# Performance work log

Measured on AMD Instinct MI355X. Metric: run time of the kernel, lower is better.

## Reference

```python
import jax, jax.numpy as jnp
import numpy as np

N_SAMPLE = 1000
N_LATENT = 64
N_OUT = 64
BATCH = 65536


def setup_inputs() -> dict:
    key = jax.random.key(0)
    k_u, k_sid, k_A, k_off = jax.random.split(key, 4)
    u = jax.random.normal(k_u, (BATCH, N_LATENT), dtype=jnp.float32)
    sample_id = jax.random.randint(k_sid, (BATCH, 1), 0, N_SAMPLE, dtype=jnp.int64)
    amat_sample = jax.random.normal(k_A, (N_SAMPLE, N_LATENT, N_OUT), dtype=jnp.float32)
    offsets = jax.random.normal(k_off, (N_SAMPLE, N_OUT), dtype=jnp.float32)
    return {"u": u, "sample_id": sample_id, "amat_sample": amat_sample, "offsets": offsets}


def reference(u, sample_id, amat_sample, offsets):
    # sample_id: [B, 1] -> [B]
    sid = jnp.squeeze(sample_id, axis=-1).astype(jnp.int32)
    # Gather per-cell decoder matrix: [B, n_latent, n_out]
    As = amat_sample[sid]
    # Original detaches u before the matvec (gradient only flows via residual).
    u_sg = jax.lax.stop_gradient(u)
    # Batched matvec: (As * u[..., None]).sum(-2)
    z2 = jnp.einsum('bd,bdo->bo', u_sg, As)
    delta = z2 + offsets[sid]
    return u + delta
```

## Files before the change

### kernel.cpp

```cpp
#include <hip/hip_runtime.h>
#include <hip/hip_bf16.h>

#define N_LATENT 64
#define N_OUT    64
#define CAP      256
#define CSTRIDE  16
#define NWAVES   5

typedef __attribute__((ext_vector_type(8))) _Float16 f16x8;
typedef __attribute__((ext_vector_type(4))) float    f32x4;

union U4H8 { uint4 u4; f16x8 h8; };

__global__ void build_lists_kernel(const int* __restrict__ sid,
                                   int* __restrict__ cursor,
                                   int* __restrict__ list,
                                   int n4)
{
    const int i = blockIdx.x * blockDim.x + threadIdx.x;
    if (i < n4) {
        const int4 v = ((const int4*)sid)[i];
        int p;
        p = atomicAdd(&cursor[v.x * CSTRIDE], 1); if (p < CAP) list[v.x * CAP + p] = 4 * i;
        p = atomicAdd(&cursor[v.y * CSTRIDE], 1); if (p < CAP) list[v.y * CAP + p] = 4 * i + 1;
        p = atomicAdd(&cursor[v.z * CSTRIDE], 1); if (p < CAP) list[v.z * CAP + p] = 4 * i + 2;
        p = atomicAdd(&cursor[v.w * CSTRIDE], 1); if (p < CAP) list[v.w * CAP + p] = 4 * i + 3;
    }
}

__global__ __launch_bounds__(64 * NWAVES) void decoder_mfma_kernel(
    const float* __restrict__ u,
    const float* __restrict__ amat,
    const float* __restrict__ offsets,
    const int*   __restrict__ cursor,
    const int*   __restrict__ list,
    float*       __restrict__ out)
{
    __shared__ uint Bf[8 * 64 * 4];

    const int s    = blockIdx.x;
    const int tid  = threadIdx.x;
    const int lane = tid & 63;
    const int wave = tid >> 6;

    int n = cursor[s * CSTRIDE];
    n = (n < CAP) ? n : CAP;
    if (n == 0) return;

    const float* __restrict__ Ag  = amat + (size_t)s * (N_LATENT * N_OUT);
    const int*   __restrict__ lst = list + s * CAP;

    for (int c = wave; c < 8; c += NWAVES) {
        const int kk  = c >> 2;
        const int nt  = c & 3;
        const int kb  = kk * 32 + (lane >> 4) * 8;
        const int col = nt * 16 + (lane & 15);
        U4H8 x;
#pragma unroll
        for (int j = 0; j < 8; ++j)
            x.h8[j] = (_Float16)Ag[(kb + j) * N_OUT + col];
        *((uint4*)&Bf[(c * 64 + lane) * 4]) = x.u4;
    }
    __syncthreads();

    const int tiles = (n + 15) >> 4;

    float off_nt[4];
#pragma unroll
    for (int nt = 0; nt < 4; ++nt)
        off_nt[nt] = offsets[(size_t)s * N_OUT + nt * 16 + (lane & 15)];

    for (int t = wave; t < tiles; t += NWAVES) {
        const int ridx = t * 16 + (lane & 15);
        const int brow = lst[(ridx < n) ? ridx : 0];
        const float* __restrict__ up =
            u + (size_t)brow * N_LATENT + ((lane >> 4) * 8);
        f16x8 a0, a1;
        {
            const float4 p0 = *(const float4*)(up);
            const float4 p1 = *(const float4*)(up + 4);
            const float4 p2 = *(const float4*)(up + 32);
            const float4 p3 = *(const float4*)(up + 36);
            a0[0] = (_Float16)p0.x; a0[1] = (_Float16)p0.y;
            a0[2] = (_Float16)p0.z; a0[3] = (_Float16)p0.w;
            a0[4] = (_Float16)p1.x; a0[5] = (_Float16)p1.y;
            a0[6] = (_Float16)p1.z; a0[7] = (_Float16)p1.w;
            a1[0] = (_Float16)p2.x; a1[1] = (_Float16)p2.y;
            a1[2] = (_Float16)p2.z; a1[3] = (_Float16)p2.w;
            a1[4] = (_Float16)p3.x; a1[5] = (_Float16)p3.y;
            a1[6] = (_Float16)p3.z; a1[7] = (_Float16)p3.w;
        }

        int  b2[4]; bool val[4];
#pragma unroll
        for (int r = 0; r < 4; ++r) {
            const int ridx2 = t * 16 + (lane >> 4) * 4 + r;
            val[r] = (ridx2 < n);
            b2[r]  = lst[val[r] ? ridx2 : 0];
        }

#pragma unroll
        for (int nt = 0; nt < 4; ++nt) {
            U4H8 b0, b1;
            b0.u4 = *((const uint4*)&Bf[((0 * 4 + nt) * 64 + lane) * 4]);
            b1.u4 = *((const uint4*)&Bf[((1 * 4 + nt) * 64 + lane) * 4]);
            f32x4 acc = {0.f, 0.f, 0.f, 0.f};
            acc = __builtin_amdgcn_mfma_f32_16x16x32_f16(a0, b0.h8, acc, 0, 0, 0);
            acc = __builtin_amdgcn_mfma_f32_16x16x32_f16(a1, b1.h8, acc, 0, 0, 0);

            const int col = nt * 16 + (lane & 15);
#pragma unroll
            for (int r = 0; r < 4; ++r) {
                if (val[r]) {
                    const size_t idx = (size_t)b2[r] * N_OUT + col;
                    out[idx] = u[idx] + acc[r] + off_nt[nt];
                }
            }
        }
    }
}

extern "C" void kernel_launch(void* const* d_in, const int* in_sizes, int n_in,
                              void* d_out, int out_size, void* d_ws, size_t ws_size,
                              hipStream_t stream)
{
    const float* u       = (const float*)d_in[0];
    const int*   sid     = (const int*)d_in[1];
    const float* amat    = (const float*)d_in[2];
    const float* offsets = (const float*)d_in[3];
    float*       out     = (float*)d_out;

    const int batch    = in_sizes[0] / N_LATENT;
    const int n_sample = in_sizes[2] / (N_LATENT * N_OUT);

    int* cursor = (int*)d_ws;
    int* list   = cursor + (size_t)n_sample * CSTRIDE;

    hipMemsetAsync(cursor, 0, (size_t)n_sample * CSTRIDE * sizeof(int), stream);

    const int n4 = batch / 4;
    build_lists_kernel<<<(n4 + 255) / 256, 256, 0, stream>>>(
        sid, cursor, list, n4);

    decoder_mfma_kernel<<<n_sample, 64 * NWAVES, 0, stream>>>(
        u, amat, offsets, cursor, list, out);
}
```

Baseline: 29.34 us.

## Stage MFMA results in LDS for coalesced float4 epilogue; one id per thread in list build

The MFMA accumulators are written into a per-wave padded LDS tile. The epilogue then reads each output row back as float4 and writes it with coalesced 16-byte loads and stores of u and out, replacing scattered 4-byte accesses. The list-building kernel now handles one sample id per thread instead of four, which spreads the atomics over more threads. The change adds LDS traffic and relies on an lgkmcnt wait with no barrier for intra-wave visibility, which should hold because each wave uses its own tile.

```diff
diff --git a/kernel.cpp b/kernel.cpp
--- a/kernel.cpp
+++ b/kernel.cpp
@@ -6,25 +6,24 @@
 #define CAP      256
 #define CSTRIDE  16
 #define NWAVES   5
+#define TPAD     68
 
 typedef __attribute__((ext_vector_type(8))) _Float16 f16x8;
 typedef __attribute__((ext_vector_type(4))) float    f32x4;
 
 union U4H8 { uint4 u4; f16x8 h8; };
 
-__global__ void build_lists_kernel(const int* __restrict__ sid,
-                                   int* __restrict__ cursor,
-                                   int* __restrict__ list,
-                                   int n4)
+__global__ __launch_bounds__(256) void build_lists_kernel(
+    const int* __restrict__ sid,
+    int* __restrict__ cursor,
+    int* __restrict__ list,
+    int batch)
 {
     const int i = blockIdx.x * blockDim.x + threadIdx.x;
-    if (i < n4) {
-        const int4 v = ((const int4*)sid)[i];
-        int p;
-        p = atomicAdd(&cursor[v.x * CSTRIDE], 1); if (p < CAP) list[v.x * CAP + p] = 4 * i;
-        p = atomicAdd(&cursor[v.y * CSTRIDE], 1); if (p < CAP) list[v.y * CAP + p] = 4 * i + 1;
-        p = atomicAdd(&cursor[v.z * CSTRIDE], 1); if (p < CAP) list[v.z * CAP + p] = 4 * i + 2;
-        p = atomicAdd(&cursor[v.w * CSTRIDE], 1); if (p < CAP) list[v.w * CAP + p] = 4 * i + 3;
+    if (i < batch) {
+        const int s = sid[i];
+        const int p = atomicAdd(&cursor[s * CSTRIDE], 1);
+        if (p < CAP) list[s * CAP + p] = i;
     }
 }
 
@@ -36,7 +35,8 @@
     const int*   __restrict__ list,
     float*       __restrict__ out)
 {
-    __shared__ uint Bf[8 * 64 * 4];
+    __shared__ uint  Bf[8 * 64 * 4];
+    __shared__ float Ot[NWAVES][16 * TPAD];
 
     const int s    = blockIdx.x;
     const int tid  = threadIdx.x;
@@ -65,10 +65,9 @@
 
     const int tiles = (n + 15) >> 4;
 
-    float off_nt[4];
-#pragma unroll
-    for (int nt = 0; nt < 4; ++nt)
-        off_nt[nt] = offsets[(size_t)s * N_OUT + nt * 16 + (lane & 15)];
+    const float4 offv = *(const float4*)(offsets + (size_t)s * N_OUT + (lane & 15) * 4);
+
+    float* __restrict__ myT = &Ot[wave][0];
 
     for (int t = wave; t < tiles; t += NWAVES) {
         const int ridx = t * 16 + (lane & 15);
@@ -91,14 +90,6 @@
             a1[6] = (_Float16)p3.z; a1[7] = (_Float16)p3.w;
         }
 
-        int  b2[4]; bool val[4];
-#pragma unroll
-        for (int r = 0; r < 4; ++r) {
-            const int ridx2 = t * 16 + (lane >> 4) * 4 + r;
-            val[r] = (ridx2 < n);
-            b2[r]  = lst[val[r] ? ridx2 : 0];
-        }
-
 #pragma unroll
         for (int nt = 0; nt < 4; ++nt) {
             U4H8 b0, b1;
@@ -110,11 +101,29 @@
 
             const int col = nt * 16 + (lane & 15);
 #pragma unroll
-            for (int r = 0; r < 4; ++r) {
-                if (val[r]) {
-                    const size_t idx = (size_t)b2[r] * N_OUT + col;
-                    out[idx] = u[idx] + acc[r] + off_nt[nt];
-                }
+            for (int r = 0; r < 4; ++r)
+                myT[((lane >> 4) * 4 + r) * TPAD + col] = acc[r];
+        }
+        asm volatile("s_waitcnt lgkmcnt(0)" ::: "memory");
+
+#pragma unroll
+        for (int p = 0; p < 4; ++p) {
+            const int r2    = p * 4 + (lane >> 4);
+            const int ridx2 = t * 16 + r2;
+            if (ridx2 < n) {
+                const int brow2 = lst[ridx2];
+                const float* __restrict__ urow =
+                    u + (size_t)brow2 * N_LATENT + (lane & 15) * 4;
+                float* __restrict__ orow =
+                    out + (size_t)brow2 * N_OUT + (lane & 15) * 4;
+                const float4 uq = *(const float4*)urow;
+                const float4 tv = *(const float4*)(myT + r2 * TPAD + (lane & 15) * 4);
+                float4 o;
+                o.x = uq.x + tv.x + offv.x;
+                o.y = uq.y + tv.y + offv.y;
+                o.z = uq.z + tv.z + offv.z;
+                o.w = uq.w + tv.w + offv.w;
+                *(float4*)orow = o;
             }
         }
     }
@@ -138,9 +147,8 @@
 
     hipMemsetAsync(cursor, 0, (size_t)n_sample * CSTRIDE * sizeof(int), stream);
 
-    const int n4 = batch / 4;
-    build_lists_kernel<<<(n4 + 255) / 256, 256, 0, stream>>>(
-        sid, cursor, list, n4);
+    build_lists_kernel<<<(batch + 255) / 256, 256, 0, stream>>>(
+        sid, cursor, list, batch);
 
     decoder_mfma_kernel<<<n_sample, 64 * NWAVES, 0, stream>>>(
         u, amat, offsets, cursor, list, out);
```

Result: faster. 25.70 us (median of 3 runs) (-12.4%).
